# Kernel tuning notes

Hardware: AMD Instinct MI355X
Metric: run time of the kernel (lower is better)

## Reference

```python
import jax, jax.numpy as jnp
import numpy as np
import math

D = 512
H = 512

def setup_inputs() -> dict:
    key = jax.random.key(0)
    k1, k2, k3, k4 = jax.random.split(key, 4)
    x = jax.random.normal(k1, (64, 1024, D), dtype=jnp.float32)
    h0 = jax.random.normal(k2, (64, H), dtype=jnp.float32)
    Wx = jax.random.normal(k3, (D, 4 * H), dtype=jnp.float32) / math.sqrt(D)
    Wh = jax.random.normal(k4, (H, 4 * H), dtype=jnp.float32) / math.sqrt(H)
    b = jnp.zeros((4 * H,), dtype=jnp.float32)
    return {"x": x, "h0": h0, "Wx": Wx, "Wh": Wh, "b": b}

def reference(x, h0, Wx, Wh, b):
    # x: (N,T,D), h0: (N,H). Precompute input projections for all steps at once.
    Hd = h0.shape[-1]
    xW = jnp.einsum('ntd,df->ntf', x, Wx) + b  # (N,T,4H)

    def step(carry, xw_t):
        h, c = carry
        A = xw_t + h @ Wh  # (N,4H)
        i = jax.nn.sigmoid(A[:, :Hd])
        f = jax.nn.sigmoid(A[:, Hd:2 * Hd])
        o = jax.nn.sigmoid(A[:, 2 * Hd:3 * Hd])
        g = jnp.tanh(A[:, 3 * Hd:])
        c_next = f * c + i * g
        h_next = o * jnp.tanh(c_next)
        return (h_next, c_next), h_next

    c0 = jnp.zeros_like(h0)
    # scan over time axis: move T to leading dim
    _, hs = jax.lax.scan(step, (h0, c0), jnp.swapaxes(xW, 0, 1))  # (T,N,H)
    return jnp.swapaxes(hs, 0, 1)  # (N,T,H)
```

## Files before the change

kernel.cpp:

```cpp
#include <hip/hip_runtime.h>
#include <hip/hip_bf16.h>
#include <math.h>


#define TT 1024
#define HH 512
#define FH 2048
#define KK 1024
#define NN 64

typedef __attribute__((ext_vector_type(8))) short bf16x8;
typedef __attribute__((ext_vector_type(4))) float f32x4;
typedef __attribute__((ext_vector_type(4))) int int4v;
typedef __attribute__((ext_vector_type(2))) int int2v;

__device__ __forceinline__ unsigned short f2bf(float f) {
    return __builtin_bit_cast(unsigned short, __float2bfloat16(f));
}

__global__ __launch_bounds__(256)
void prep_wt(const float* __restrict__ Wx, const float* __restrict__ Wh,
             unsigned short* __restrict__ Wt)
{
    __shared__ float tile[64][65];
    const int c0  = blockIdx.x * 64;
    const int k0  = blockIdx.y * 64;
    const int tid = threadIdx.x;

    #pragma unroll
    for (int it = 0; it < 16; ++it) {
        int idx = it * 256 + tid;
        int kk = idx >> 6, cc = idx & 63;
        int k = k0 + kk;
        float w = (k < 512) ? Wx[(size_t)k * FH + c0 + cc]
                            : Wh[(size_t)(k - 512) * FH + c0 + cc];
        tile[kk][cc] = w;
    }
    __syncthreads();

    #pragma unroll
    for (int it = 0; it < 8; ++it) {
        int idx = it * 256 + tid;
        int cc = idx >> 5, kp = idx & 31;
        unsigned int lo = f2bf(tile[kp * 2][cc]);
        unsigned int hi = f2bf(tile[kp * 2 + 1][cc]);
        *(unsigned int*)(Wt + (size_t)(c0 + cc) * KK + k0 + kp * 2) =
            lo | (hi << 16);
    }
}

__global__ __launch_bounds__(256)
void lstm_init(const float* __restrict__ h0,
               unsigned short* __restrict__ hb,
               unsigned int* __restrict__ flg)
{
    int id = blockIdx.x * 256 + threadIdx.x;
    if (id < 256 * 16) {
        unsigned int* p = flg + id;
        unsigned int z = 0u;
        asm volatile("global_store_dword %0, %1, off sc0 sc1" :: "v"(p), "v"(z) : "memory");
    }
    if (id < NN * HH) {
        unsigned int hv = (unsigned int)f2bf(h0[id]);
        unsigned short* hp = hb + id;
        asm volatile("global_store_short %0, %1, off sc0 sc1" :: "v"(hp), "v"(hv) : "memory");
    }
}

__global__ __launch_bounds__(512)
void lstm_persist(const float* __restrict__ x,
                  const unsigned short* __restrict__ Wt,
                  const float* __restrict__ bias,
                  float* __restrict__ out,
                  unsigned short* __restrict__ hb,
                  unsigned int* __restrict__ flg)
{
    __shared__ __align__(16) unsigned short Aph[16 * 512];
    __shared__ float part[8][16][17];

    const int tid  = threadIdx.x;
    const int wv   = tid >> 6;
    const int lane = tid & 63;
    const int l15  = lane & 15;
    const int kh   = lane >> 4;

    const int rg = blockIdx.x >> 6;
    const int jg = blockIdx.x & 63;
    const int j0 = jg * 8;
    const int rowbase = rg * 16;

    const int ct = wv & 1;
    const int kq = wv >> 1;

    const int lc   = ct * 16 + l15;
    const int gate = lc >> 3;
    const int jj   = lc & 7;
    const int gcol = gate * HH + j0 + jj;

    const unsigned short* wtp = Wt + (size_t)gcol * KK + kh * 8;
    bf16x8 bx[4], bh[4];
    #pragma unroll
    for (int ks = 0; ks < 4; ++ks) {
        bx[ks] = *(const bf16x8*)(wtp + kq * 128 + ks * 32);
        bh[ks] = *(const bf16x8*)(wtp + 512 + kq * 128 + ks * 32);
    }

    const float* xlane = x + (size_t)(rowbase + l15) * TT * 512 + kq * 128 + kh * 8;

    const int arow = l15;
    const int rsw  = ((arow & 15) << 3) | ((arow & 3) << 7);

    const int srow  = tid >> 5;
    const int scol  = tid & 31;
    const int rsw_s = ((srow & 15) << 3) | ((srow & 3) << 7);
    const unsigned short* hrow = hb + (size_t)(rowbase + srow) * HH + scol * 16;
    unsigned short* aps0 = Aph + srow * 512 + ((scol * 16) ^ rsw_s);
    unsigned short* aps1 = Aph + srow * 512 + (((scol * 16) + 8) ^ rsw_s);

    const int grow_l = (tid >> 3) & 15;
    const int q      = tid & 7;
    const int grow   = rowbase + grow_l;
    const int gj     = j0 + q;
    float bi = 0.f, bf_ = 0.f, bo = 0.f, bg = 0.f;
    if (tid < 128) {
        bi  = bias[gj];
        bf_ = bias[HH + gj];
        bo  = bias[2 * HH + gj];
        bg  = bias[3 * HH + gj];
    }
    float c_reg = 0.f;
    float* outp = out + (size_t)grow * TT * HH + gj;
    unsigned short* hdst0 = hb + (size_t)grow * HH + gj;

    unsigned int* myflag = flg + (size_t)blockIdx.x * 16 + wv;
    const unsigned int* pollp = flg + (size_t)(rg * 64 + lane) * 16;

    int4v xw[8];
    {
        #pragma unroll
        for (int ks = 0; ks < 4; ++ks) {
            asm volatile("global_load_dwordx4 %0, %1, off" : "=v"(xw[2 * ks])     : "v"(xlane + ks * 32));
            asm volatile("global_load_dwordx4 %0, %1, off" : "=v"(xw[2 * ks + 1]) : "v"(xlane + ks * 32 + 4));
        }
        asm volatile("s_waitcnt vmcnt(0)" ::: "memory");
        __builtin_amdgcn_sched_barrier(0);
    }
    bf16x8 xf[4];
    #pragma unroll
    for (int ks = 0; ks < 4; ++ks) {
        float4 u = __builtin_bit_cast(float4, xw[2 * ks]);
        float4 v = __builtin_bit_cast(float4, xw[2 * ks + 1]);
        bf16x8 a;
        a[0] = (short)f2bf(u.x); a[1] = (short)f2bf(u.y);
        a[2] = (short)f2bf(u.z); a[3] = (short)f2bf(u.w);
        a[4] = (short)f2bf(v.x); a[5] = (short)f2bf(v.y);
        a[6] = (short)f2bf(v.z); a[7] = (short)f2bf(v.w);
        xf[ks] = a;
    }

    for (int t = 0; t < TT; ++t) {
        const int pb  = t & 1;
        const int nxt = pb ^ 1;

        f32x4 accx = {0.f, 0.f, 0.f, 0.f};
        #pragma unroll
        for (int ks = 0; ks < 4; ++ks)
            accx = __builtin_amdgcn_mfma_f32_16x16x32_bf16(xf[ks], bx[ks], accx, 0, 0, 0);

        if (t > 0 && wv == 0) {
            const unsigned int tgt = (unsigned int)t;
            int2v v;
            do {
                asm volatile("global_load_dwordx2 %0, %1, off sc0 sc1\n\t"
                             "s_waitcnt vmcnt(0)"
                             : "=v"(v) : "v"(pollp) : "memory");
            } while (!__all(((unsigned int)v[0] >= tgt) & ((unsigned int)v[1] >= tgt)));
        }
        __syncthreads();

        {
            const unsigned short* hs = hrow + (size_t)pb * NN * HH;
            int4v h0v, h1v;
            asm volatile("global_load_dwordx4 %0, %2, off sc0 sc1\n\t"
                         "global_load_dwordx4 %1, %3, off sc0 sc1\n\t"
                         "s_waitcnt vmcnt(0)"
                         : "=&v"(h0v), "=&v"(h1v)
                         : "v"(hs), "v"(hs + 8) : "memory");
            __builtin_amdgcn_sched_barrier(0);
            *(int4v*)aps0 = h0v;
            *(int4v*)aps1 = h1v;
        }
        __syncthreads();

        f32x4 acch = {0.f, 0.f, 0.f, 0.f};
        #pragma unroll
        for (int ks = 0; ks < 4; ++ks) {
            bf16x8 hf = *(const bf16x8*)(Aph + arow * 512
                           + ((kq * 128 + ks * 32 + kh * 8) ^ rsw));
            acch = __builtin_amdgcn_mfma_f32_16x16x32_bf16(hf, bh[ks], acch, 0, 0, 0);
        }
        #pragma unroll
        for (int rr = 0; rr < 4; ++rr)
            part[wv][kh * 4 + rr][l15] = accx[rr] + acch[rr];
        __syncthreads();

        if (tid < 128) {
            float Ai = bi, Af = bf_, Ao = bo, Ag = bg;
            #pragma unroll
            for (int k2 = 0; k2 < 4; ++k2) {
                Ai += part[2 * k2][grow_l][q];
                Af += part[2 * k2][grow_l][8 + q];
                Ao += part[2 * k2 + 1][grow_l][q];
                Ag += part[2 * k2 + 1][grow_l][8 + q];
            }
            float ig = 1.f / (1.f + __expf(-Ai));
            float fg = 1.f / (1.f + __expf(-Af));
            float og = 1.f / (1.f + __expf(-Ao));
            float eg = __expf(2.f * Ag);
            float gg = 1.f - 2.f / (eg + 1.f);
            c_reg = fg * c_reg + ig * gg;
            float ec = __expf(2.f * c_reg);
            float tc = 1.f - 2.f / (ec + 1.f);
            float hn = og * tc;

            unsigned int hv = (unsigned int)f2bf(hn);
            unsigned short* hdst = hdst0 + (size_t)nxt * NN * HH;
            asm volatile("global_store_short %0, %1, off sc0 sc1"
                         :: "v"(hdst), "v"(hv) : "memory");
            asm volatile("s_waitcnt vmcnt(0)" ::: "memory");
            if (t + 1 < TT && lane == 0) {
                unsigned int tgt2 = (unsigned int)(t + 1);
                asm volatile("global_store_dword %0, %1, off sc0 sc1"
                             :: "v"(myflag), "v"(tgt2) : "memory");
            }
            outp[(size_t)t * HH] = hn;
        }

        if (t + 1 < TT) {
            const float* xp = xlane + (size_t)(t + 1) * 512;
            #pragma unroll
            for (int ks = 0; ks < 4; ++ks) {
                asm volatile("global_load_dwordx4 %0, %1, off" : "=v"(xw[2 * ks])     : "v"(xp + ks * 32));
                asm volatile("global_load_dwordx4 %0, %1, off" : "=v"(xw[2 * ks + 1]) : "v"(xp + ks * 32 + 4));
            }
            asm volatile("s_waitcnt vmcnt(0)" ::: "memory");
            __builtin_amdgcn_sched_barrier(0);
            #pragma unroll
            for (int ks = 0; ks < 4; ++ks) {
                float4 u = __builtin_bit_cast(float4, xw[2 * ks]);
                float4 v = __builtin_bit_cast(float4, xw[2 * ks + 1]);
                bf16x8 a;
                a[0] = (short)f2bf(u.x); a[1] = (short)f2bf(u.y);
                a[2] = (short)f2bf(u.z); a[3] = (short)f2bf(u.w);
                a[4] = (short)f2bf(v.x); a[5] = (short)f2bf(v.y);
                a[6] = (short)f2bf(v.z); a[7] = (short)f2bf(v.w);
                xf[ks] = a;
            }
        }
    }
}

extern "C" void kernel_launch(void* const* d_in, const int* in_sizes, int n_in,
                              void* d_out, int out_size, void* d_ws, size_t ws_size,
                              hipStream_t stream)
{
    const float* x  = (const float*)d_in[0];
    const float* h0 = (const float*)d_in[1];
    const float* Wx = (const float*)d_in[2];
    const float* Wh = (const float*)d_in[3];
    const float* b  = (const float*)d_in[4];
    float* out = (float*)d_out;

    char* ws = (char*)d_ws;
    unsigned short* Wt  = (unsigned short*)ws;
    unsigned short* hb  = (unsigned short*)(ws + (size_t)4 * 1024 * 1024);
    unsigned int*   flg = (unsigned int*)(ws + (size_t)4 * 1024 * 1024 + 131072);

    prep_wt<<<dim3(32, 16), 256, 0, stream>>>(Wx, Wh, Wt);
    lstm_init<<<128, 256, 0, stream>>>(h0, hb, flg);
    lstm_persist<<<256, 512, 0, stream>>>(x, Wt, b, out, hb, flg);
}
```

Before: 3.187 ms.

## Fuse step tag into hidden-state words to replace flag polling

Each hidden-state value now sits in a 32-bit word with the bf16 value in the low half and the timestep tag in the high half. Consumers poll the h buffer directly until every tag matches the current step, then pack the values into LDS. This drops the separate flag array, the store-wait-then-flag sequence on the producer side, and one block barrier plus the dedicated polling wave per step. In exchange the h buffer is twice as large, every thread spins on its own loads, and the design relies on each 32-bit store being seen atomically.

Measured after the change: 3.186 ms. No clear change (-0.0%).

```diff
diff --git a/kernel.cpp b/kernel.cpp
--- a/kernel.cpp
+++ b/kernel.cpp
@@ -12,7 +12,7 @@
 typedef __attribute__((ext_vector_type(8))) short bf16x8;
 typedef __attribute__((ext_vector_type(4))) float f32x4;
 typedef __attribute__((ext_vector_type(4))) int int4v;
-typedef __attribute__((ext_vector_type(2))) int int2v;
+typedef __attribute__((ext_vector_type(2))) unsigned int uint2v;
 
 __device__ __forceinline__ unsigned short f2bf(float f) {
     return __builtin_bit_cast(unsigned short, __float2bfloat16(f));
@@ -50,20 +50,16 @@
 }
 
 __global__ __launch_bounds__(256)
-void lstm_init(const float* __restrict__ h0,
-               unsigned short* __restrict__ hb,
-               unsigned int* __restrict__ flg)
+void lstm_init(const float* __restrict__ h0, unsigned int* __restrict__ hb32)
 {
     int id = blockIdx.x * 256 + threadIdx.x;
-    if (id < 256 * 16) {
-        unsigned int* p = flg + id;
-        unsigned int z = 0u;
-        asm volatile("global_store_dword %0, %1, off sc0 sc1" :: "v"(p), "v"(z) : "memory");
-    }
     if (id < NN * HH) {
-        unsigned int hv = (unsigned int)f2bf(h0[id]);
-        unsigned short* hp = hb + id;
-        asm volatile("global_store_short %0, %1, off sc0 sc1" :: "v"(hp), "v"(hv) : "memory");
+        unsigned int v0 = (unsigned int)f2bf(h0[id]);
+        unsigned int v1 = 0xFFFF0000u;
+        unsigned int* p0 = hb32 + id;
+        unsigned int* p1 = hb32 + NN * HH + id;
+        asm volatile("global_store_dword %0, %1, off sc0 sc1" :: "v"(p0), "v"(v0) : "memory");
+        asm volatile("global_store_dword %0, %1, off sc0 sc1" :: "v"(p1), "v"(v1) : "memory");
     }
 }
 
@@ -72,8 +68,7 @@
                   const unsigned short* __restrict__ Wt,
                   const float* __restrict__ bias,
                   float* __restrict__ out,
-                  unsigned short* __restrict__ hb,
-                  unsigned int* __restrict__ flg)
+                  unsigned int* __restrict__ hb32)
 {
     __shared__ __align__(16) unsigned short Aph[16 * 512];
     __shared__ float part[8][16][17];
@@ -113,9 +108,7 @@
     const int srow  = tid >> 5;
     const int scol  = tid & 31;
     const int rsw_s = ((srow & 15) << 3) | ((srow & 3) << 7);
-    const unsigned short* hrow = hb + (size_t)(rowbase + srow) * HH + scol * 16;
-    unsigned short* aps0 = Aph + srow * 512 + ((scol * 16) ^ rsw_s);
-    unsigned short* aps1 = Aph + srow * 512 + (((scol * 16) + 8) ^ rsw_s);
+    const unsigned int* hrow32 = hb32 + (size_t)(rowbase + srow) * HH + scol * 4;
 
     const int grow_l = (tid >> 3) & 15;
     const int q      = tid & 7;
@@ -130,10 +123,7 @@
     }
     float c_reg = 0.f;
     float* outp = out + (size_t)grow * TT * HH + gj;
-    unsigned short* hdst0 = hb + (size_t)grow * HH + gj;
-
-    unsigned int* myflag = flg + (size_t)blockIdx.x * 16 + wv;
-    const unsigned int* pollp = flg + (size_t)(rg * 64 + lane) * 16;
+    unsigned int* hdst32 = hb32 + (size_t)grow * HH + gj;
 
     int4v xw[8];
     {
@@ -159,36 +149,51 @@
     }
 
     for (int t = 0; t < TT; ++t) {
-        const int pb  = t & 1;
-        const int nxt = pb ^ 1;
+        const int pb = t & 1;
+        const unsigned int tg = (unsigned int)t;
+        const unsigned int* hp = hrow32 + (size_t)pb * NN * HH;
+
+        int4v hw[4];
+        #pragma unroll
+        for (int i = 0; i < 4; ++i) {
+            asm volatile("global_load_dwordx4 %0, %1, off sc0 sc1"
+                         : "=v"(hw[i]) : "v"(hp + i * 128));
+        }
 
         f32x4 accx = {0.f, 0.f, 0.f, 0.f};
         #pragma unroll
         for (int ks = 0; ks < 4; ++ks)
             accx = __builtin_amdgcn_mfma_f32_16x16x32_bf16(xf[ks], bx[ks], accx, 0, 0, 0);
 
-        if (t > 0 && wv == 0) {
-            const unsigned int tgt = (unsigned int)t;
-            int2v v;
-            do {
-                asm volatile("global_load_dwordx2 %0, %1, off sc0 sc1\n\t"
-                             "s_waitcnt vmcnt(0)"
-                             : "=v"(v) : "v"(pollp) : "memory");
-            } while (!__all(((unsigned int)v[0] >= tgt) & ((unsigned int)v[1] >= tgt)));
-        }
-        __syncthreads();
-
-        {
-            const unsigned short* hs = hrow + (size_t)pb * NN * HH;
-            int4v h0v, h1v;
-            asm volatile("global_load_dwordx4 %0, %2, off sc0 sc1\n\t"
-                         "global_load_dwordx4 %1, %3, off sc0 sc1\n\t"
-                         "s_waitcnt vmcnt(0)"
-                         : "=&v"(h0v), "=&v"(h1v)
-                         : "v"(hs), "v"(hs + 8) : "memory");
+        asm volatile("s_waitcnt vmcnt(0)" ::: "memory");
+        __builtin_amdgcn_sched_barrier(0);
+        while (true) {
+            int ok = 1;
+            #pragma unroll
+            for (int i = 0; i < 4; ++i) {
+                #pragma unroll
+                for (int e = 0; e < 4; ++e)
+                    ok &= (int)((((unsigned int)hw[i][e]) >> 16) == tg);
+            }
+            if (__all(ok)) break;
+            if (!ok) {
+                #pragma unroll
+                for (int i = 0; i < 4; ++i) {
+                    asm volatile("global_load_dwordx4 %0, %1, off sc0 sc1"
+                                 : "=v"(hw[i]) : "v"(hp + i * 128));
+                }
+            }
+            asm volatile("s_waitcnt vmcnt(0)" ::: "memory");
             __builtin_amdgcn_sched_barrier(0);
-            *(int4v*)aps0 = h0v;
-            *(int4v*)aps1 = h1v;
+        }
+
+        #pragma unroll
+        for (int i = 0; i < 4; ++i) {
+            unsigned int lo = ((unsigned int)hw[i][0] & 0xFFFFu) | ((unsigned int)hw[i][1] << 16);
+            unsigned int hi = ((unsigned int)hw[i][2] & 0xFFFFu) | ((unsigned int)hw[i][3] << 16);
+            int s = (i * 128 + scol * 4) ^ rsw_s;
+            uint2v pk = {lo, hi};
+            *(uint2v*)(Aph + srow * 512 + s) = pk;
         }
         __syncthreads();
 
@@ -223,16 +228,10 @@
             float tc = 1.f - 2.f / (ec + 1.f);
             float hn = og * tc;
 
-            unsigned int hv = (unsigned int)f2bf(hn);
-            unsigned short* hdst = hdst0 + (size_t)nxt * NN * HH;
-            asm volatile("global_store_short %0, %1, off sc0 sc1"
+            unsigned int hv = (((unsigned int)(t + 1)) << 16) | (unsigned int)f2bf(hn);
+            unsigned int* hdst = hdst32 + (size_t)((t + 1) & 1) * NN * HH;
+            asm volatile("global_store_dword %0, %1, off sc0 sc1"
                          :: "v"(hdst), "v"(hv) : "memory");
-            asm volatile("s_waitcnt vmcnt(0)" ::: "memory");
-            if (t + 1 < TT && lane == 0) {
-                unsigned int tgt2 = (unsigned int)(t + 1);
-                asm volatile("global_store_dword %0, %1, off sc0 sc1"
-                             :: "v"(myflag), "v"(tgt2) : "memory");
-            }
             outp[(size_t)t * HH] = hn;
         }
 
@@ -272,11 +271,10 @@
     float* out = (float*)d_out;
 
     char* ws = (char*)d_ws;
-    unsigned short* Wt  = (unsigned short*)ws;
-    unsigned short* hb  = (unsigned short*)(ws + (size_t)4 * 1024 * 1024);
-    unsigned int*   flg = (unsigned int*)(ws + (size_t)4 * 1024 * 1024 + 131072);
+    unsigned short* Wt   = (unsigned short*)ws;
+    unsigned int*   hb32 = (unsigned int*)(ws + (size_t)4 * 1024 * 1024);
 
     prep_wt<<<dim3(32, 16), 256, 0, stream>>>(Wx, Wh, Wt);
-    lstm_init<<<128, 256, 0, stream>>>(h0, hb, flg);
-    lstm_persist<<<256, 512, 0, stream>>>(x, Wt, b, out, hb, flg);
-}
+    lstm_init<<<128, 256, 0, stream>>>(h0, hb32);
+    lstm_persist<<<256, 512, 0, stream>>>(x, Wt, b, out, hb32);
+}
```
